# Kernel optimization log

Hardware: AMD Instinct MI355X
Metric: run time of the kernel (lower is better)

The kernel has to match this reference:

```python
import jax, jax.numpy as jnp
import numpy as np

D_MODEL = 256; D_FLOW = 128; D_FFN = 1024
N_HEADS = 8; N_LEVELS = 3; N_POINTS = 4
D_HEAD = D_MODEL // N_HEADS
SHAPES = np.array([[128, 128], [64, 64], [32, 32]], dtype=np.int64)


def setup_inputs():
    key = jax.random.key(0)
    ks = jax.random.split(key, 12)
    N = 2
    LeNin = int((SHAPES[:, 0] * SHAPES[:, 1]).sum())
    Lq = int(SHAPES[0, 0] * SHAPES[0, 1])
    lsi = np.concatenate([[0], np.cumsum(SHAPES[:, 0] * SHAPES[:, 1])[:-1]])
    s = 0.02
    return {
        'src': jax.random.normal(ks[0], (N, LeNin, D_MODEL), jnp.float32),
        'flow': jax.random.normal(ks[1], (N, Lq, D_FLOW), jnp.float32),
        'spatial_shapes': jnp.asarray(SHAPES, jnp.int32),
        'level_start_index': jnp.asarray(lsi, jnp.int32),
        'w_value': jax.random.normal(ks[2], (D_MODEL, D_MODEL), jnp.float32) * s,
        'b_value': jnp.zeros((D_MODEL,), jnp.float32),
        'w_off': jax.random.normal(ks[3], (D_FLOW, N_HEADS * N_LEVELS * N_POINTS * 2), jnp.float32) * s,
        'b_off': jax.random.normal(ks[4], (N_HEADS * N_LEVELS * N_POINTS * 2,), jnp.float32) * 0.5,
        'w_attn': jax.random.normal(ks[5], (D_FLOW, N_HEADS * N_LEVELS * N_POINTS), jnp.float32) * s,
        'b_attn': jnp.zeros((N_HEADS * N_LEVELS * N_POINTS,), jnp.float32),
        'w_out': jax.random.normal(ks[6], (D_MODEL, D_MODEL), jnp.float32) * s,
        'b_out': jnp.zeros((D_MODEL,), jnp.float32),
        'gamma': jnp.ones((D_MODEL,), jnp.float32),
        'beta': jnp.zeros((D_MODEL,), jnp.float32),
        'w1': jax.random.normal(ks[7], (D_MODEL, D_FFN), jnp.float32) * s,
        'b1': jnp.zeros((D_FFN,), jnp.float32),
        'w2': jax.random.normal(ks[8], (D_FFN, D_MODEL), jnp.float32) * s,
        'b2': jnp.zeros((D_MODEL,), jnp.float32),
    }


def _bilinear_level(v, xy, H, W):
    # v: [N, nh, H*W, dh]; xy: [N, Lq, nh, np, 2] normalized to [0,1]
    # grid_sample(align_corners=False) semantics: pixel = loc * size - 0.5, zero padding
    N, Lq = xy.shape[0], xy.shape[1]
    x = xy[..., 0] * W - 0.5
    y = xy[..., 1] * H - 0.5
    x0 = jnp.floor(x); y0 = jnp.floor(y)
    dx = x - x0; dy = y - y0
    acc = jnp.zeros((N, N_HEADS, Lq * N_POINTS, v.shape[-1]), v.dtype)
    corners = ((x0, y0, (1 - dx) * (1 - dy)),
               (x0 + 1, y0, dx * (1 - dy)),
               (x0, y0 + 1, (1 - dx) * dy),
               (x0 + 1, y0 + 1, dx * dy))
    for ix, iy, w in corners:
        valid = (ix >= 0) & (ix <= W - 1) & (iy >= 0) & (iy <= H - 1)
        xi = jnp.clip(ix, 0, W - 1).astype(jnp.int32)
        yi = jnp.clip(iy, 0, H - 1).astype(jnp.int32)
        idx = (yi * W + xi).transpose(0, 2, 1, 3).reshape(N, N_HEADS, Lq * N_POINTS)
        g = jnp.take_along_axis(v, idx[..., None], axis=2)  # [N, nh, Lq*np, dh]
        wv = (w * valid).transpose(0, 2, 1, 3).reshape(N, N_HEADS, Lq * N_POINTS, 1)
        acc = acc + wv * g
    return acc


def reference(src, flow, spatial_shapes, level_start_index, w_value, b_value,
              w_off, b_off, w_attn, b_attn, w_out, b_out, gamma, beta, w1, b1, w2, b2):
    ss = np.asarray(jax.device_get(spatial_shapes))
    lsi = np.asarray(jax.device_get(level_start_index))
    N, LeNin, _ = src.shape
    Lq = flow.shape[1]
    value = (src @ w_value + b_value).reshape(N, LeNin, N_HEADS, D_HEAD)
    off = (flow @ w_off + b_off).reshape(N, Lq, N_HEADS, N_LEVELS, N_POINTS, 2)
    attn = jax.nn.softmax((flow @ w_attn + b_attn).reshape(N, Lq, N_HEADS, N_LEVELS * N_POINTS), axis=-1)
    attn = attn.reshape(N, Lq, N_HEADS, N_LEVELS, N_POINTS)
    # reference points on level-0 grid (valid_ratios == 1)
    H0, W0 = int(ss[0, 0]), int(ss[0, 1])
    ry, rx = jnp.meshgrid(jnp.linspace(0.5, H0 - 0.5, H0) / H0,
                          jnp.linspace(0.5, W0 - 0.5, W0) / W0, indexing='ij')
    ref = jnp.stack([rx.reshape(-1), ry.reshape(-1)], -1)  # [Lq, 2] (x, y)
    norm = jnp.asarray(np.stack([ss[:, 1], ss[:, 0]], -1), jnp.float32)  # [nl, 2] = (W, H)
    loc = ref[None, :, None, None, None, :] + off / norm[None, None, None, :, None, :]
    acc = jnp.zeros((N, Lq, N_HEADS, D_HEAD), src.dtype)
    for l in range(N_LEVELS):
        H, W = int(ss[l, 0]), int(ss[l, 1])
        st = int(lsi[l])
        v = value[:, st:st + H * W].transpose(0, 2, 1, 3)  # [N, nh, HW, dh]
        s_l = _bilinear_level(v, loc[:, :, :, l], H, W).reshape(N, N_HEADS, Lq, N_POINTS, D_HEAD)
        acc = acc + jnp.einsum('bhqpd,bqhp->bqhd', s_l, attn[:, :, :, l])
    src2 = acc.reshape(N, Lq, D_MODEL) @ w_out + b_out
    x = src2  # dropout is identity at inference
    mu = x.mean(-1, keepdims=True)
    var = ((x - mu) ** 2).mean(-1, keepdims=True)
    ln = (x - mu) / jnp.sqrt(var + 1e-5) * gamma + beta
    ffn = jax.nn.relu(ln @ w1 + b1) @ w2 + b2
    return x + ffn
```

## Files before the change

### kernel.cpp

```cpp
#include <hip/hip_runtime.h>
#include <cstdint>
#include <cstddef>

#define D_MODEL  256
#define D_FLOW   128
#define D_FFN    1024
#define N_HEADS  8
#define N_LEVELS 3
#define N_POINTS 4
#define D_HEAD   32
#define LQ       16384
#define LENIN    21504
#define NB       2

typedef unsigned short ushort;
typedef __attribute__((ext_vector_type(8))) short bf16x8;
typedef __attribute__((ext_vector_type(4))) float f32x4;

__device__ __forceinline__ ushort f2b(float f) {
    uint32_t u = __float_as_uint(f);
    uint32_t r = (u + 0x7fffu + ((u >> 16) & 1u)) >> 16;
    return (ushort)r;
}

__device__ __forceinline__ void gl_lds16(const void* g, void* l) {
    __builtin_amdgcn_global_load_lds(
        (const __attribute__((address_space(1))) unsigned int*)g,
        (__attribute__((address_space(3))) unsigned int*)l,
        16, 0, 0);
}

template<bool RELU, bool RESID, bool OUT_BF16>
__global__ __launch_bounds__(256)
void mfma_gemm(const ushort* __restrict__ A, const ushort* __restrict__ Bt,
               const float* __restrict__ bias, const float* __restrict__ resid,
               void* __restrict__ Cout, int N, int K)
{
    __shared__ ushort As[128 * 32];
    __shared__ ushort Bs[128 * 32];

    const int tid  = threadIdx.x;
    const int wave = tid >> 6;
    const int lane = tid & 63;
    const int quad = lane >> 4;
    const int l16  = lane & 15;
    const int wr   = (wave >> 1) * 64;
    const int wc   = (wave & 1) * 64;
    const int bm   = blockIdx.y * 128;
    const int bn   = blockIdx.x * 128;

    const int sr   = lane >> 2;
    const int sc   = lane & 3;
    const int gch  = sc ^ (sr & 3);
    const int row0 = wave * 32 + sr;
    const int row1 = row0 + 16;

    const ushort* pA0 = A  + (size_t)(bm + row0) * K + gch * 8;
    const ushort* pA1 = A  + (size_t)(bm + row1) * K + gch * 8;
    const ushort* pB0 = Bt + (size_t)(bn + row0) * K + gch * 8;
    const ushort* pB1 = Bt + (size_t)(bn + row1) * K + gch * 8;
    ushort* lA0 = As + wave * 1024;
    ushort* lA1 = As + wave * 1024 + 512;
    ushort* lB0 = Bs + wave * 1024;
    ushort* lB1 = Bs + wave * 1024 + 512;

    f32x4 acc[4][4] = {};
    const int swz = l16 & 3;

    for (int k0 = 0; k0 < K; k0 += 32) {
        __syncthreads();
        gl_lds16(pA0 + k0, lA0);
        gl_lds16(pA1 + k0, lA1);
        gl_lds16(pB0 + k0, lB0);
        gl_lds16(pB1 + k0, lB1);
        __syncthreads();

        bf16x8 af[4], bfr[4];
#pragma unroll
        for (int mi = 0; mi < 4; ++mi)
            af[mi] = *(const bf16x8*)&As[(wr + mi * 16 + l16) * 32 + ((quad ^ swz) << 3)];
#pragma unroll
        for (int ni = 0; ni < 4; ++ni)
            bfr[ni] = *(const bf16x8*)&Bs[(wc + ni * 16 + l16) * 32 + ((quad ^ swz) << 3)];
#pragma unroll
        for (int mi = 0; mi < 4; ++mi)
#pragma unroll
            for (int ni = 0; ni < 4; ++ni)
                acc[mi][ni] = __builtin_amdgcn_mfma_f32_16x16x32_bf16(
                    af[mi], bfr[ni], acc[mi][ni], 0, 0, 0);
    }

#pragma unroll
    for (int mi = 0; mi < 4; ++mi) {
#pragma unroll
        for (int ni = 0; ni < 4; ++ni) {
            const int col = bn + wc + ni * 16 + l16;
            const float bb = bias[col];
#pragma unroll
            for (int r = 0; r < 4; ++r) {
                const int row = bm + wr + mi * 16 + quad * 4 + r;
                const size_t idx = (size_t)row * N + col;
                float c = acc[mi][ni][r] + bb;
                if (RELU)  c = fmaxf(c, 0.f);
                if (RESID) c += resid[idx];
                if (OUT_BF16) ((ushort*)Cout)[idx] = f2b(c);
                else          ((float*)Cout)[idx]  = c;
            }
        }
    }
}

__device__ __forceinline__ void acc8(float* a, uint4 g, float w) {
    a[0] = fmaf(w, __uint_as_float(g.x << 16), a[0]);
    a[1] = fmaf(w, __uint_as_float(g.x & 0xffff0000u), a[1]);
    a[2] = fmaf(w, __uint_as_float(g.y << 16), a[2]);
    a[3] = fmaf(w, __uint_as_float(g.y & 0xffff0000u), a[3]);
    a[4] = fmaf(w, __uint_as_float(g.z << 16), a[4]);
    a[5] = fmaf(w, __uint_as_float(g.z & 0xffff0000u), a[5]);
    a[6] = fmaf(w, __uint_as_float(g.w << 16), a[6]);
    a[7] = fmaf(w, __uint_as_float(g.w & 0xffff0000u), a[7]);
}

__global__ __launch_bounds__(256)
void sample_k(const ushort* __restrict__ value, const ushort* __restrict__ projc,
              ushort* __restrict__ acc)
{
    __shared__ float sOff[8][192];
    __shared__ float sAttn[8][96];

    const int tid = threadIdx.x;
    const int bq0 = blockIdx.x * 8;

    for (int i = tid; i < 8 * 288; i += 256) {
        const int qw = i / 288, j = i - qw * 288;
        const float v = __uint_as_float((uint32_t)projc[(size_t)(bq0 + qw) * 384 + j] << 16);
        if (j < 192) sOff[qw][j] = v;
        else         sAttn[qw][j - 192] = v;
    }
    __syncthreads();

    if (tid < 64) {
        const int qw = tid >> 3, h = tid & 7;
        float* row = &sAttn[qw][h * 12];
        float m = row[0];
#pragma unroll
        for (int j = 1; j < 12; ++j) m = fmaxf(m, row[j]);
        float s = 0.f;
#pragma unroll
        for (int j = 0; j < 12; ++j) { const float e = __expf(row[j] - m); row[j] = e; s += e; }
        const float inv = 1.f / s;
#pragma unroll
        for (int j = 0; j < 12; ++j) row[j] *= inv;
    }
    __syncthreads();

    const int wave = tid >> 6, lane = tid & 63;
    const int qh = lane >> 5;
    const int h  = (lane >> 2) & 7;
    const int cg = lane & 3;
    const int qw = wave * 2 + qh;
    const int bq = bq0 + qw;
    const int n  = bq >> 14;
    const int q  = bq & 16383;

    const float qx = (float)(q & 127) + 0.5f;
    const float qy = (float)(q >> 7) + 0.5f;

    const int LSIc[3] = {0, 16384, 20480};

    float a[8] = {0.f, 0.f, 0.f, 0.f, 0.f, 0.f, 0.f, 0.f};
    const ushort* vbase = value + (size_t)n * LENIN * D_MODEL + h * D_HEAD + cg * 8;

#pragma unroll
    for (int l = 0; l < N_LEVELS; ++l) {
        const int   W     = 128 >> l;
        const int   SH    = 7 - l;
        const float scale = 1.f / (float)(1 << l);
        const float cx    = qx * scale - 0.5f;
        const float cy    = qy * scale - 0.5f;
        const ushort* vlev = vbase + ((size_t)LSIc[l] << 8);
#pragma unroll
        for (int p = 0; p < N_POINTS; ++p) {
            const int ob = (h * N_LEVELS + l) * (N_POINTS * 2) + p * 2;
            const float aw = sAttn[qw][h * 12 + l * 4 + p];
            const float x = cx + sOff[qw][ob];
            const float y = cy + sOff[qw][ob + 1];
            const float x0f = floorf(x), y0f = floorf(y);
            const int x0 = (int)x0f, y0 = (int)y0f;
            const float dx = x - x0f, dy = y - y0f;
            float wx1 = dx * aw, wx0 = aw - wx1;
            float wy1 = dy,      wy0 = 1.f - dy;
            if ((unsigned)x0       > (unsigned)(W - 1)) wx0 = 0.f;
            if ((unsigned)(x0 + 1) > (unsigned)(W - 1)) wx1 = 0.f;
            if ((unsigned)y0       > (unsigned)(W - 1)) wy0 = 0.f;
            if ((unsigned)(y0 + 1) > (unsigned)(W - 1)) wy1 = 0.f;
            const int xi0 = min(max(x0, 0), W - 1);
            const int xi1 = min(max(x0 + 1, 0), W - 1);
            const int yi0 = min(max(y0, 0), W - 1);
            const int yi1 = min(max(y0 + 1, 0), W - 1);
            const uint4 g00 = *(const uint4*)(vlev + ((size_t)((yi0 << SH) + xi0) << 8));
            const uint4 g01 = *(const uint4*)(vlev + ((size_t)((yi0 << SH) + xi1) << 8));
            const uint4 g10 = *(const uint4*)(vlev + ((size_t)((yi1 << SH) + xi0) << 8));
            const uint4 g11 = *(const uint4*)(vlev + ((size_t)((yi1 << SH) + xi1) << 8));
            acc8(a, g00, wx0 * wy0);
            acc8(a, g01, wx1 * wy0);
            acc8(a, g10, wx0 * wy1);
            acc8(a, g11, wx1 * wy1);
        }
    }

    const uint32_t o0 = (uint32_t)f2b(a[0]) | ((uint32_t)f2b(a[1]) << 16);
    const uint32_t o1 = (uint32_t)f2b(a[2]) | ((uint32_t)f2b(a[3]) << 16);
    const uint32_t o2 = (uint32_t)f2b(a[4]) | ((uint32_t)f2b(a[5]) << 16);
    const uint32_t o3 = (uint32_t)f2b(a[6]) | ((uint32_t)f2b(a[7]) << 16);
    const uint4 ov = {o0, o1, o2, o3};
    *(uint4*)(acc + (size_t)bq * D_MODEL + h * D_HEAD + cg * 8) = ov;
}

__global__ __launch_bounds__(256)
void ln_k(const float* __restrict__ x, const float* __restrict__ gamma,
          const float* __restrict__ beta, ushort* __restrict__ out)
{
    const int wave = threadIdx.x >> 6;
    const int lane = threadIdx.x & 63;
    const size_t row = (size_t)blockIdx.x * 4 + wave;

    const float4 v = *(const float4*)(x + row * 256 + lane * 4);
    float s  = v.x + v.y + v.z + v.w;
    float s2 = v.x * v.x + v.y * v.y + v.z * v.z + v.w * v.w;
#pragma unroll
    for (int off = 32; off > 0; off >>= 1) {
        s  += __shfl_xor(s, off);
        s2 += __shfl_xor(s2, off);
    }
    const float mu  = s * (1.f / 256.f);
    const float var = s2 * (1.f / 256.f) - mu * mu;
    const float r   = rsqrtf(var + 1e-5f);

    const float4 g = *(const float4*)(gamma + lane * 4);
    const float4 b = *(const float4*)(beta + lane * 4);
    ushort4 o;
    o.x = f2b((v.x - mu) * r * g.x + b.x);
    o.y = f2b((v.y - mu) * r * g.y + b.y);
    o.z = f2b((v.z - mu) * r * g.z + b.z);
    o.w = f2b((v.w - mu) * r * g.w + b.w);
    *(ushort4*)(out + row * 256 + lane * 4) = o;
}

__global__ __launch_bounds__(256)
void f2b_k(const float* __restrict__ x, ushort* __restrict__ y, int n4)
{
    const int i = blockIdx.x * 256 + threadIdx.x;
    if (i < n4) {
        const float4 v = ((const float4*)x)[i];
        ushort4 o = { f2b(v.x), f2b(v.y), f2b(v.z), f2b(v.w) };
        ((ushort4*)y)[i] = o;
    }
}

__global__ __launch_bounds__(256)
void tconv_k(const float* __restrict__ w, ushort* __restrict__ wT, int K, int N)
{
    const int i = blockIdx.x * 256 + threadIdx.x;
    if (i < K * N) {
        const int k = i / N, n = i - k * N;
        wT[(size_t)n * K + k] = f2b(w[i]);
    }
}

__global__ __launch_bounds__(256)
void prep_proj_k(const float* __restrict__ w_off, const float* __restrict__ b_off,
                 const float* __restrict__ w_attn, const float* __restrict__ b_attn,
                 ushort* __restrict__ wT, float* __restrict__ biasc)
{
    const int i = blockIdx.x * 256 + threadIdx.x;
    if (i < 384 * 128) {
        const int nn = i >> 7, k = i & 127;
        float v = 0.f;
        if (nn < 192)      v = w_off[(size_t)k * 192 + nn];
        else if (nn < 288) v = w_attn[(size_t)k * 96 + (nn - 192)];
        wT[i] = f2b(v);
    }
    if (i < 384) {
        float b = 0.f;
        if (i < 192)      b = b_off[i];
        else if (i < 288) b = b_attn[i - 192];
        biasc[i] = b;
    }
}

extern "C" void kernel_launch(void* const* d_in, const int* in_sizes, int n_in,
                              void* d_out, int out_size, void* d_ws, size_t ws_size,
                              hipStream_t stream)
{
    const float* src     = (const float*)d_in[0];
    const float* flow    = (const float*)d_in[1];
    const float* w_value = (const float*)d_in[4];
    const float* b_value = (const float*)d_in[5];
    const float* w_off   = (const float*)d_in[6];
    const float* b_off   = (const float*)d_in[7];
    const float* w_attn  = (const float*)d_in[8];
    const float* b_attn  = (const float*)d_in[9];
    const float* w_out   = (const float*)d_in[10];
    const float* b_out   = (const float*)d_in[11];
    const float* gamma   = (const float*)d_in[12];
    const float* beta    = (const float*)d_in[13];
    const float* w1      = (const float*)d_in[14];
    const float* b1      = (const float*)d_in[15];
    const float* w2      = (const float*)d_in[16];
    const float* b2      = (const float*)d_in[17];
    float* out = (float*)d_out;
    char*  wsb = (char*)d_ws;

    ushort* src_bf   = (ushort*)(wsb);
    ushort* flow_bf  = (ushort*)(wsb + 22020096);
    ushort* acc_bf   = (ushort*)(wsb + 30408704);
    ushort* ffn1_bf  = (ushort*)(wsb);
    ushort* value_bf = (ushort*)(wsb + 67108864);
    ushort* ln_bf    = (ushort*)(wsb + 67108864);
    ushort* projc_bf = (ushort*)(wsb + 89128960);
    ushort* wvT      = (ushort*)(wsb + 114294784);
    ushort* woT      = (ushort*)(wsb + 114425856);
    ushort* w1T      = (ushort*)(wsb + 114556928);
    ushort* w2T      = (ushort*)(wsb + 115081216);
    ushort* wcT      = (ushort*)(wsb + 115605504);
    float*  biasc    = (float*) (wsb + 115703808);

    const int Mq = NB * LQ;
    const int Mv = NB * LENIN;

    f2b_k<<<(Mv * 256 / 4 + 255) / 256, 256, 0, stream>>>(src, src_bf, Mv * 256 / 4);
    f2b_k<<<(Mq * 128 / 4 + 255) / 256, 256, 0, stream>>>(flow, flow_bf, Mq * 128 / 4);
    tconv_k<<<(256 * 256 + 255) / 256, 256, 0, stream>>>(w_value, wvT, 256, 256);
    tconv_k<<<(256 * 256 + 255) / 256, 256, 0, stream>>>(w_out,  woT, 256, 256);
    tconv_k<<<(256 * 1024 + 255) / 256, 256, 0, stream>>>(w1, w1T, 256, 1024);
    tconv_k<<<(1024 * 256 + 255) / 256, 256, 0, stream>>>(w2, w2T, 1024, 256);
    prep_proj_k<<<192, 256, 0, stream>>>(w_off, b_off, w_attn, b_attn, wcT, biasc);

    mfma_gemm<false, false, true><<<dim3(2, Mv / 128), 256, 0, stream>>>(
        src_bf, wvT, b_value, nullptr, value_bf, 256, 256);

    mfma_gemm<false, false, true><<<dim3(3, Mq / 128), 256, 0, stream>>>(
        flow_bf, wcT, biasc, nullptr, projc_bf, 384, 128);

    sample_k<<<Mq / 8, 256, 0, stream>>>(value_bf, projc_bf, acc_bf);

    mfma_gemm<false, false, false><<<dim3(2, Mq / 128), 256, 0, stream>>>(
        acc_bf, woT, b_out, nullptr, out, 256, 256);

    ln_k<<<Mq / 4, 256, 0, stream>>>(out, gamma, beta, ln_bf);

    mfma_gemm<true, false, true><<<dim3(8, Mq / 128), 256, 0, stream>>>(
        ln_bf, w1T, b1, nullptr, ffn1_bf, 1024, 256);

    mfma_gemm<false, true, false><<<dim3(2, Mq / 128), 256, 0, stream>>>(
        ffn1_bf, w2T, b2, out, out, 256, 1024);
}
```

Measured before the change: 312.1 us.

## Fuse fp32-to-bf16 input conversion into GEMM loads and widen K tile to 64

The separate f2b conversion kernels for src and flow are removed. The GEMM now reads fp32 A directly, converts it to bf16 in registers and stores it to LDS, which avoids writing and re-reading a bf16 copy of src and flow. The K tile grows from 32 to 64 with an 8-way XOR swizzle, halving the number of barrier pairs per K loop at the cost of twice the LDS. The fp32 A path uses plain register loads instead of direct-to-LDS loads, which may add latency, and the fp32 A tile is converted again by each N-block that reads it.

```diff
diff --git a/kernel.cpp b/kernel.cpp
--- a/kernel.cpp
+++ b/kernel.cpp
@@ -30,14 +30,14 @@
         16, 0, 0);
 }
 
-template<bool RELU, bool RESID, bool OUT_BF16>
-__global__ __launch_bounds__(256)
-void mfma_gemm(const ushort* __restrict__ A, const ushort* __restrict__ Bt,
+template<bool A_FP32, bool RELU, bool RESID, bool OUT_BF16>
+__global__ __launch_bounds__(256)
+void mfma_gemm(const void* __restrict__ Ain, const ushort* __restrict__ Bt,
                const float* __restrict__ bias, const float* __restrict__ resid,
                void* __restrict__ Cout, int N, int K)
 {
-    __shared__ ushort As[128 * 32];
-    __shared__ ushort Bs[128 * 32];
+    __shared__ ushort As[128 * 64];
+    __shared__ ushort Bs[128 * 64];
 
     const int tid  = threadIdx.x;
     const int wave = tid >> 6;
@@ -49,45 +49,67 @@
     const int bm   = blockIdx.y * 128;
     const int bn   = blockIdx.x * 128;
 
-    const int sr   = lane >> 2;
-    const int sc   = lane & 3;
-    const int gch  = sc ^ (sr & 3);
-    const int row0 = wave * 32 + sr;
-    const int row1 = row0 + 16;
-
-    const ushort* pA0 = A  + (size_t)(bm + row0) * K + gch * 8;
-    const ushort* pA1 = A  + (size_t)(bm + row1) * K + gch * 8;
-    const ushort* pB0 = Bt + (size_t)(bn + row0) * K + gch * 8;
-    const ushort* pB1 = Bt + (size_t)(bn + row1) * K + gch * 8;
-    ushort* lA0 = As + wave * 1024;
-    ushort* lA1 = As + wave * 1024 + 512;
-    ushort* lB0 = Bs + wave * 1024;
-    ushort* lB1 = Bs + wave * 1024 + 512;
+    const int sr  = lane >> 3;
+    const int sc  = lane & 7;
+    const int gch = sc ^ sr;
 
     f32x4 acc[4][4] = {};
-    const int swz = l16 & 3;
-
-    for (int k0 = 0; k0 < K; k0 += 32) {
+    const int swz = l16 & 7;
+
+    for (int k0 = 0; k0 < K; k0 += 64) {
         __syncthreads();
-        gl_lds16(pA0 + k0, lA0);
-        gl_lds16(pA1 + k0, lA1);
-        gl_lds16(pB0 + k0, lB0);
-        gl_lds16(pB1 + k0, lB1);
+        if (A_FP32) {
+            const float* Af = (const float*)Ain;
+#pragma unroll
+            for (int i = 0; i < 4; ++i) {
+                const int row = wave * 32 + i * 8 + sr;
+                const float* p = Af + (size_t)(bm + row) * K + k0 + gch * 8;
+                const float4 v0 = *(const float4*)(p);
+                const float4 v1 = *(const float4*)(p + 4);
+                bf16x8 pk;
+                pk[0] = (short)f2b(v0.x); pk[1] = (short)f2b(v0.y);
+                pk[2] = (short)f2b(v0.z); pk[3] = (short)f2b(v0.w);
+                pk[4] = (short)f2b(v1.x); pk[5] = (short)f2b(v1.y);
+                pk[6] = (short)f2b(v1.z); pk[7] = (short)f2b(v1.w);
+                *(bf16x8*)&As[(size_t)row * 64 + sc * 8] = pk;
+            }
+        } else {
+            const ushort* Ab = (const ushort*)Ain;
+#pragma unroll
+            for (int i = 0; i < 4; ++i) {
+                const int row = wave * 32 + i * 8;
+                gl_lds16(Ab + (size_t)(bm + row + sr) * K + k0 + gch * 8,
+                         As + (size_t)row * 64);
+            }
+        }
+#pragma unroll
+        for (int i = 0; i < 4; ++i) {
+            const int row = wave * 32 + i * 8;
+            gl_lds16(Bt + (size_t)(bn + row + sr) * K + k0 + gch * 8,
+                     Bs + (size_t)row * 64);
+        }
         __syncthreads();
 
-        bf16x8 af[4], bfr[4];
-#pragma unroll
-        for (int mi = 0; mi < 4; ++mi)
-            af[mi] = *(const bf16x8*)&As[(wr + mi * 16 + l16) * 32 + ((quad ^ swz) << 3)];
-#pragma unroll
-        for (int ni = 0; ni < 4; ++ni)
-            bfr[ni] = *(const bf16x8*)&Bs[(wc + ni * 16 + l16) * 32 + ((quad ^ swz) << 3)];
-#pragma unroll
-        for (int mi = 0; mi < 4; ++mi)
-#pragma unroll
-            for (int ni = 0; ni < 4; ++ni)
-                acc[mi][ni] = __builtin_amdgcn_mfma_f32_16x16x32_bf16(
-                    af[mi], bfr[ni], acc[mi][ni], 0, 0, 0);
+#pragma unroll
+        for (int kk = 0; kk < 2; ++kk) {
+            bf16x8 af[4], bfr[4];
+#pragma unroll
+            for (int mi = 0; mi < 4; ++mi) {
+                const int p = (kk * 4 + quad) ^ swz;
+                af[mi] = *(const bf16x8*)&As[(wr + mi * 16 + l16) * 64 + p * 8];
+            }
+#pragma unroll
+            for (int ni = 0; ni < 4; ++ni) {
+                const int p = (kk * 4 + quad) ^ swz;
+                bfr[ni] = *(const bf16x8*)&Bs[(wc + ni * 16 + l16) * 64 + p * 8];
+            }
+#pragma unroll
+            for (int mi = 0; mi < 4; ++mi)
+#pragma unroll
+                for (int ni = 0; ni < 4; ++ni)
+                    acc[mi][ni] = __builtin_amdgcn_mfma_f32_16x16x32_bf16(
+                        af[mi], bfr[ni], acc[mi][ni], 0, 0, 0);
+        }
     }
 
 #pragma unroll
@@ -248,17 +270,6 @@
 }
 
 __global__ __launch_bounds__(256)
-void f2b_k(const float* __restrict__ x, ushort* __restrict__ y, int n4)
-{
-    const int i = blockIdx.x * 256 + threadIdx.x;
-    if (i < n4) {
-        const float4 v = ((const float4*)x)[i];
-        ushort4 o = { f2b(v.x), f2b(v.y), f2b(v.z), f2b(v.w) };
-        ((ushort4*)y)[i] = o;
-    }
-}
-
-__global__ __launch_bounds__(256)
 void tconv_k(const float* __restrict__ w, ushort* __restrict__ wT, int K, int N)
 {
     const int i = blockIdx.x * 256 + threadIdx.x;
@@ -312,47 +323,43 @@
     float* out = (float*)d_out;
     char*  wsb = (char*)d_ws;
 
-    ushort* src_bf   = (ushort*)(wsb);
-    ushort* flow_bf  = (ushort*)(wsb + 22020096);
-    ushort* acc_bf   = (ushort*)(wsb + 30408704);
     ushort* ffn1_bf  = (ushort*)(wsb);
-    ushort* value_bf = (ushort*)(wsb + 67108864);
+    ushort* value_bf = (ushort*)(wsb);
+    ushort* acc_bf   = (ushort*)(wsb + 22020096);
+    ushort* projc_bf = (ushort*)(wsb + 67108864);
     ushort* ln_bf    = (ushort*)(wsb + 67108864);
-    ushort* projc_bf = (ushort*)(wsb + 89128960);
-    ushort* wvT      = (ushort*)(wsb + 114294784);
-    ushort* woT      = (ushort*)(wsb + 114425856);
-    ushort* w1T      = (ushort*)(wsb + 114556928);
-    ushort* w2T      = (ushort*)(wsb + 115081216);
-    ushort* wcT      = (ushort*)(wsb + 115605504);
-    float*  biasc    = (float*) (wsb + 115703808);
+    ushort* wvT      = (ushort*)(wsb + 92274688);
+    ushort* woT      = (ushort*)(wsb + 92405760);
+    ushort* w1T      = (ushort*)(wsb + 92536832);
+    ushort* w2T      = (ushort*)(wsb + 93061120);
+    ushort* wcT      = (ushort*)(wsb + 93585408);
+    float*  biasc    = (float*) (wsb + 93683712);
 
     const int Mq = NB * LQ;
     const int Mv = NB * LENIN;
 
-    f2b_k<<<(Mv * 256 / 4 + 255) / 256, 256, 0, stream>>>(src, src_bf, Mv * 256 / 4);
-    f2b_k<<<(Mq * 128 / 4 + 255) / 256, 256, 0, stream>>>(flow, flow_bf, Mq * 128 / 4);
     tconv_k<<<(256 * 256 + 255) / 256, 256, 0, stream>>>(w_value, wvT, 256, 256);
     tconv_k<<<(256 * 256 + 255) / 256, 256, 0, stream>>>(w_out,  woT, 256, 256);
     tconv_k<<<(256 * 1024 + 255) / 256, 256, 0, stream>>>(w1, w1T, 256, 1024);
     tconv_k<<<(1024 * 256 + 255) / 256, 256, 0, stream>>>(w2, w2T, 1024, 256);
     prep_proj_k<<<192, 256, 0, stream>>>(w_off, b_off, w_attn, b_attn, wcT, biasc);
 
-    mfma_gemm<false, false, true><<<dim3(2, Mv / 128), 256, 0, stream>>>(
-        src_bf, wvT, b_value, nullptr, value_bf, 256, 256);
-
-    mfma_gemm<false, false, true><<<dim3(3, Mq / 128), 256, 0, stream>>>(
-        flow_bf, wcT, biasc, nullptr, projc_bf, 384, 128);
+    mfma_gemm<true, false, false, true><<<dim3(2, Mv / 128), 256, 0, stream>>>(
+        src, wvT, b_value, nullptr, value_bf, 256, 256);
+
+    mfma_gemm<true, false, false, true><<<dim3(3, Mq / 128), 256, 0, stream>>>(
+        flow, wcT, biasc, nullptr, projc_bf, 384, 128);
 
     sample_k<<<Mq / 8, 256, 0, stream>>>(value_bf, projc_bf, acc_bf);
 
-    mfma_gemm<false, false, false><<<dim3(2, Mq / 128), 256, 0, stream>>>(
+    mfma_gemm<false, false, false, false><<<dim3(2, Mq / 128), 256, 0, stream>>>(
         acc_bf, woT, b_out, nullptr, out, 256, 256);
 
     ln_k<<<Mq / 4, 256, 0, stream>>>(out, gamma, beta, ln_bf);
 
-    mfma_gemm<true, false, true><<<dim3(8, Mq / 128), 256, 0, stream>>>(
+    mfma_gemm<false, true, false, true><<<dim3(8, Mq / 128), 256, 0, stream>>>(
         ln_bf, w1T, b1, nullptr, ffn1_bf, 1024, 256);
 
-    mfma_gemm<false, true, false><<<dim3(2, Mq / 128), 256, 0, stream>>>(
+    mfma_gemm<false, false, true, false><<<dim3(2, Mq / 128), 256, 0, stream>>>(
         ffn1_bf, w2T, b2, out, out, 256, 1024);
 }
```

After: 308.8 us. No clear change (-1.1%).
